# Performance work log

Measured on AMD Instinct MI355X. Metric: run time of the kernel, lower is better.

## Reference

```python
import jax, jax.numpy as jnp
import numpy as np

D_HEAD = 64
SCALE = D_HEAD ** 0.5
MASK_FILL = -10000.0


def setup_inputs() -> dict:
    key = jax.random.key(0)
    kq, kk, kv, km = jax.random.split(key, 4)
    B, H, S, D = 2, 16, 2048, D_HEAD
    query = jax.random.normal(kq, (B, H, S, D), dtype=jnp.float32)
    k = jax.random.normal(kk, (B, H, S, D), dtype=jnp.float32)
    v = jax.random.normal(kv, (B, H, S, D), dtype=jnp.float32)
    attn_mask = jax.random.randint(km, (B, H, S, S), 0, 2).astype(jnp.bool_)
    return {"query": query, "key": k, "value": v, "attn_mask": attn_mask}


def reference(query, key, value, attn_mask):
    # scores: [B, H, Sq, Sk]
    scores = jnp.einsum("bhqd,bhkd->bhqk", query, key) / SCALE
    scores = jnp.where(attn_mask, MASK_FILL, scores)
    attn_prob = jax.nn.softmax(scores, axis=-1)
    context = jnp.einsum("bhqk,bhkd->bhqd", attn_prob, value)
    return (context, attn_prob)
```

## Files before the change

### kernel.cpp

```cpp
#include <hip/hip_runtime.h>
#include <cstdint>
#include <cstddef>

#define S_LEN 2048
#define D_HEAD 64
#define NBH 32

typedef __attribute__((ext_vector_type(8))) short short8;
typedef __attribute__((ext_vector_type(8))) unsigned short ushort8;
typedef __attribute__((ext_vector_type(4))) float floatx4;

__device__ __forceinline__ unsigned short f2bf(float f){
  union { float f; unsigned int i; } v; v.f = f;
  unsigned int u = v.i;
  u += 0x7fffu + ((u >> 16) & 1u);
  return (unsigned short)(u >> 16);
}
__device__ __forceinline__ float bf2f(unsigned short u){
  union { unsigned int i; float f; } v; v.i = ((unsigned int)u) << 16; return v.f;
}

__device__ __forceinline__ int swz(int row, int col){
  return row * S_LEN + ((((col >> 3) ^ row) & 7) << 3) + ((col >> 3) & ~7) * 8 + (col & 7);
}

__global__ void detect_mask_kernel(const unsigned int* __restrict__ m, int* __restrict__ flag){
  __shared__ int f;
  if (threadIdx.x == 0) f = 0;
  __syncthreads();
  if (m[threadIdx.x] > 1u) atomicOr(&f, 1);
  __syncthreads();
  if (threadIdx.x == 0) *flag = f;
}

__global__ void convK_kernel(const float* __restrict__ K, unsigned short* __restrict__ Kb){
  const size_t i = ((size_t)blockIdx.x * 256 + threadIdx.x) * 8;
  floatx4 x0 = *(const floatx4*)(K + i);
  floatx4 x1 = *(const floatx4*)(K + i + 4);
  ushort8 o;
#pragma unroll
  for (int j = 0; j < 4; ++j){ o[j] = f2bf(x0[j]); o[4 + j] = f2bf(x1[j]); }
  *(ushort8*)(Kb + i) = o;
}

__global__ void vtrans_kernel(const float* __restrict__ V, unsigned short* __restrict__ Vt){
  const int bh = blockIdx.y;
  const int n  = threadIdx.x & 63;
  const int k0 = blockIdx.x * 32 + (threadIdx.x >> 6) * 8;
  const float* Vp = V + (size_t)bh * S_LEN * D_HEAD;
  ushort8 o;
#pragma unroll
  for (int i = 0; i < 8; ++i) o[i] = f2bf(Vp[(size_t)(k0 + i) * D_HEAD + n]);
  *(ushort8*)(Vt + (size_t)bh * D_HEAD * S_LEN + (size_t)n * S_LEN + k0) = o;
}

__global__ __launch_bounds__(256) void attn_kernel(
    const float* __restrict__ Q, const unsigned short* __restrict__ Kb,
    const void* __restrict__ maskp, const int* __restrict__ flag,
    const unsigned short* __restrict__ Vt,
    float* __restrict__ prob, float* __restrict__ ctx,
    float* __restrict__ redg, float* __restrict__ invg){

  __shared__ unsigned short Pt[16 * S_LEN];

  const int bh   = blockIdx.y;
  const int qt   = blockIdx.x;
  const int q0g  = bh * S_LEN + qt * 16;
  const int tid  = threadIdx.x;
  const int wave = tid >> 6;
  const int lane = tid & 63;
  const int quad = lane >> 4;
  const int r16  = lane & 15;
  const int blk  = bh * gridDim.x + qt;

  const float* qrow = Q + (size_t)(q0g + r16) * D_HEAD + quad * 8;
  short8 a0, a1;
  {
    floatx4 x0 = *(const floatx4*)(qrow);
    floatx4 x1 = *(const floatx4*)(qrow + 4);
    floatx4 y0 = *(const floatx4*)(qrow + 32);
    floatx4 y1 = *(const floatx4*)(qrow + 36);
#pragma unroll
    for (int j = 0; j < 4; ++j){
      a0[j] = (short)f2bf(x0[j]); a0[4 + j] = (short)f2bf(x1[j]);
      a1[j] = (short)f2bf(y0[j]); a1[4 + j] = (short)f2bf(y1[j]);
    }
  }

  const bool mInt = (*flag) == 0;
  const unsigned int*  mI = (const unsigned int*)maskp;
  const unsigned char* mB = (const unsigned char*)maskp;

  float racc[4] = {0.f, 0.f, 0.f, 0.f};

  for (int t = 0; t < 32; ++t){
    const int s0 = wave * 512 + t * 16;
    const unsigned short* krow = Kb + (size_t)(bh * S_LEN + s0 + r16) * D_HEAD + quad * 8;
    const short8 b0 = *(const short8*)(krow);
    const short8 b1 = *(const short8*)(krow + 32);
    unsigned int mv[4];
    if (mInt){
#pragma unroll
      for (int i = 0; i < 4; ++i)
        mv[i] = mI[(size_t)(q0g + quad*4 + i) * S_LEN + s0 + r16];
    } else {
#pragma unroll
      for (int i = 0; i < 4; ++i)
        mv[i] = mB[(size_t)(q0g + quad*4 + i) * S_LEN + s0 + r16];
    }
    floatx4 c = {0.f, 0.f, 0.f, 0.f};
    c = __builtin_amdgcn_mfma_f32_16x16x32_bf16(a0, b0, c, 0, 0, 0);
    c = __builtin_amdgcn_mfma_f32_16x16x32_bf16(a1, b1, c, 0, 0, 0);
#pragma unroll
    for (int i = 0; i < 4; ++i){
      const float p = mv[i] ? 0.0f : __expf(c[i] * 0.125f);
      racc[i] += p;
      Pt[swz(quad*4 + i, s0 + r16)] = f2bf(p);
    }
  }

#pragma unroll
  for (int off = 8; off; off >>= 1){
#pragma unroll
    for (int i = 0; i < 4; ++i) racc[i] += __shfl_xor(racc[i], off, 16);
  }
  if (r16 == 0){
#pragma unroll
    for (int i = 0; i < 4; ++i) redg[(size_t)blk * 64 + wave * 16 + quad*4 + i] = racc[i];
  }
  __syncthreads();
  if (tid < 16){
    float s = 0.f;
#pragma unroll
    for (int w = 0; w < 4; ++w) s += redg[(size_t)blk * 64 + w * 16 + tid];
    invg[(size_t)blk * 16 + tid] = (s > 0.f) ? (1.0f / s) : 0.0f;
  }
  __syncthreads();

  float inv4[4];
#pragma unroll
  for (int i = 0; i < 4; ++i) inv4[i] = invg[(size_t)blk * 16 + quad*4 + i];

  const unsigned short* vrow = Vt + (size_t)bh * D_HEAD * S_LEN
                                  + (size_t)(wave * 16 + r16) * S_LEN + quad * 8;
  floatx4 c = {0.f, 0.f, 0.f, 0.f};
  for (int kk = 0; kk < 64; ++kk){
    const short8 b = *(const short8*)(vrow + kk * 32);
    const short8 a = *(const short8*)(&Pt[swz(r16, kk * 32 + quad * 8)]);
    c = __builtin_amdgcn_mfma_f32_16x16x32_bf16(a, b, c, 0, 0, 0);
  }
#pragma unroll
  for (int i = 0; i < 4; ++i)
    ctx[(size_t)(q0g + quad*4 + i) * D_HEAD + wave * 16 + r16] = c[i] * inv4[i];

#pragma unroll
  for (int rr = 0; rr < 4; ++rr){
    const int row = wave * 4 + rr;
    const float iv = invg[(size_t)blk * 16 + row];
    float* pg = prob + (size_t)(q0g + row) * S_LEN;
    for (int j = 0; j < 32; ++j){
      const int col = j * 64 + lane;
      pg[col] = bf2f(Pt[swz(row, col)]) * iv;
    }
  }
}

extern "C" void kernel_launch(void* const* d_in, const int* in_sizes, int n_in,
                              void* d_out, int out_size, void* d_ws, size_t ws_size,
                              hipStream_t stream) {
  const float* Q = (const float*)d_in[0];
  const float* K = (const float*)d_in[1];
  const float* V = (const float*)d_in[2];
  const void*  M = d_in[3];

  float* ctx  = (float*)d_out;
  float* prob = (float*)d_out + (size_t)NBH * S_LEN * D_HEAD;

  int*   flag = (int*)d_ws;
  float* redg = (float*)((char*)d_ws + (1u << 12));
  float* invg = (float*)((char*)d_ws + (1u << 12) + (1u << 20));
  unsigned short* Kb = (unsigned short*)((char*)d_ws + (2u << 20));
  unsigned short* Vt = (unsigned short*)((char*)d_ws + (10u << 20));

  hipLaunchKernelGGL(detect_mask_kernel, dim3(1), dim3(256), 0, stream,
                     (const unsigned int*)M, flag);
  hipLaunchKernelGGL(convK_kernel, dim3(2048), dim3(256), 0, stream, K, Kb);
  hipLaunchKernelGGL(vtrans_kernel, dim3(S_LEN/32, NBH), dim3(256), 0, stream, V, Vt);
  hipLaunchKernelGGL(attn_kernel, dim3(S_LEN/16, NBH), dim3(256), 0, stream,
                     Q, Kb, M, flag, Vt, prob, ctx, redg, invg);
}
```

Before: 1.083 ms.

## Vectorize mask loads and probability stores, transpose MFMA operands, remap blocks per XCD

The QK^T MFMA now takes its operands swapped, so each lane owns one query row and four consecutive keys. This lets the mask be read as one 16-byte vector (or one 4-byte word for byte masks) per row instead of four strided scalar loads. Probabilities are written to LDS as 4-wide packed stores under a widened 16-way swizzle, and the final probability output is written with 8-wide LDS reads and float4 global stores. Blocks are remapped so each XCD works on a fixed group of heads for K/V cache locality, and launch bounds and unroll pragmas are added. The risks are LDS bank conflicts under the new swizzle and register pressure from the unrolling.

```diff
diff --git a/kernel.cpp b/kernel.cpp
--- a/kernel.cpp
+++ b/kernel.cpp
@@ -8,6 +8,8 @@
 
 typedef __attribute__((ext_vector_type(8))) short short8;
 typedef __attribute__((ext_vector_type(8))) unsigned short ushort8;
+typedef __attribute__((ext_vector_type(4))) unsigned short us4;
+typedef __attribute__((ext_vector_type(4))) unsigned int ui4;
 typedef __attribute__((ext_vector_type(4))) float floatx4;
 
 __device__ __forceinline__ unsigned short f2bf(float f){
@@ -21,7 +23,8 @@
 }
 
 __device__ __forceinline__ int swz(int row, int col){
-  return row * S_LEN + ((((col >> 3) ^ row) & 7) << 3) + ((col >> 3) & ~7) * 8 + (col & 7);
+  return row * S_LEN + ((((col >> 3) ^ row) & 15) << 3)
+                     + (((col >> 3) & ~15) << 3) + (col & 7);
 }
 
 __global__ void detect_mask_kernel(const unsigned int* __restrict__ m, int* __restrict__ flag){
@@ -54,7 +57,7 @@
   *(ushort8*)(Vt + (size_t)bh * D_HEAD * S_LEN + (size_t)n * S_LEN + k0) = o;
 }
 
-__global__ __launch_bounds__(256) void attn_kernel(
+__global__ __launch_bounds__(256, 2) void attn_kernel(
     const float* __restrict__ Q, const unsigned short* __restrict__ Kb,
     const void* __restrict__ maskp, const int* __restrict__ flag,
     const unsigned short* __restrict__ Vt,
@@ -63,8 +66,12 @@
 
   __shared__ unsigned short Pt[16 * S_LEN];
 
-  const int bh   = blockIdx.y;
-  const int qt   = blockIdx.x;
+  const int lin  = blockIdx.y * gridDim.x + blockIdx.x;
+  const int xcd  = lin & 7;
+  const int sub  = lin >> 3;
+  const int bh   = xcd * 4 + (sub & 3);
+  const int qt   = sub >> 2;
+
   const int q0g  = bh * S_LEN + qt * 16;
   const int tid  = threadIdx.x;
   const int wave = tid >> 6;
@@ -90,44 +97,42 @@
   const bool mInt = (*flag) == 0;
   const unsigned int*  mI = (const unsigned int*)maskp;
   const unsigned char* mB = (const unsigned char*)maskp;
-
-  float racc[4] = {0.f, 0.f, 0.f, 0.f};
-
+  const size_t mrow = (size_t)(q0g + r16) * S_LEN;
+
+  float racc = 0.f;
+
+#pragma unroll 2
   for (int t = 0; t < 32; ++t){
     const int s0 = wave * 512 + t * 16;
     const unsigned short* krow = Kb + (size_t)(bh * S_LEN + s0 + r16) * D_HEAD + quad * 8;
     const short8 b0 = *(const short8*)(krow);
     const short8 b1 = *(const short8*)(krow + 32);
-    unsigned int mv[4];
+    unsigned int mm[4];
     if (mInt){
-#pragma unroll
-      for (int i = 0; i < 4; ++i)
-        mv[i] = mI[(size_t)(q0g + quad*4 + i) * S_LEN + s0 + r16];
+      const ui4 m4 = *(const ui4*)(mI + mrow + s0 + quad * 4);
+#pragma unroll
+      for (int i = 0; i < 4; ++i) mm[i] = m4[i];
     } else {
-#pragma unroll
-      for (int i = 0; i < 4; ++i)
-        mv[i] = mB[(size_t)(q0g + quad*4 + i) * S_LEN + s0 + r16];
+      const unsigned int mv = *(const unsigned int*)(mB + mrow + s0 + quad * 4);
+#pragma unroll
+      for (int i = 0; i < 4; ++i) mm[i] = (mv >> (8 * i)) & 0xffu;
     }
     floatx4 c = {0.f, 0.f, 0.f, 0.f};
-    c = __builtin_amdgcn_mfma_f32_16x16x32_bf16(a0, b0, c, 0, 0, 0);
-    c = __builtin_amdgcn_mfma_f32_16x16x32_bf16(a1, b1, c, 0, 0, 0);
+    c = __builtin_amdgcn_mfma_f32_16x16x32_bf16(b0, a0, c, 0, 0, 0);
+    c = __builtin_amdgcn_mfma_f32_16x16x32_bf16(b1, a1, c, 0, 0, 0);
+    us4 w;
 #pragma unroll
     for (int i = 0; i < 4; ++i){
-      const float p = mv[i] ? 0.0f : __expf(c[i] * 0.125f);
-      racc[i] += p;
-      Pt[swz(quad*4 + i, s0 + r16)] = f2bf(p);
-    }
-  }
-
-#pragma unroll
-  for (int off = 8; off; off >>= 1){
-#pragma unroll
-    for (int i = 0; i < 4; ++i) racc[i] += __shfl_xor(racc[i], off, 16);
-  }
-  if (r16 == 0){
-#pragma unroll
-    for (int i = 0; i < 4; ++i) redg[(size_t)blk * 64 + wave * 16 + quad*4 + i] = racc[i];
-  }
+      const float p = mm[i] ? 0.0f : __expf(c[i] * 0.125f);
+      racc += p;
+      w[i] = f2bf(p);
+    }
+    *(us4*)(&Pt[swz(r16, s0 + quad * 4)]) = w;
+  }
+
+  racc += __shfl_xor(racc, 16);
+  racc += __shfl_xor(racc, 32);
+  if (lane < 16) redg[(size_t)blk * 64 + wave * 16 + lane] = racc;
   __syncthreads();
   if (tid < 16){
     float s = 0.f;
@@ -139,11 +144,12 @@
 
   float inv4[4];
 #pragma unroll
-  for (int i = 0; i < 4; ++i) inv4[i] = invg[(size_t)blk * 16 + quad*4 + i];
+  for (int i = 0; i < 4; ++i) inv4[i] = invg[(size_t)blk * 16 + quad * 4 + i];
 
   const unsigned short* vrow = Vt + (size_t)bh * D_HEAD * S_LEN
                                   + (size_t)(wave * 16 + r16) * S_LEN + quad * 8;
   floatx4 c = {0.f, 0.f, 0.f, 0.f};
+#pragma unroll 4
   for (int kk = 0; kk < 64; ++kk){
     const short8 b = *(const short8*)(vrow + kk * 32);
     const short8 a = *(const short8*)(&Pt[swz(r16, kk * 32 + quad * 8)]);
@@ -151,16 +157,25 @@
   }
 #pragma unroll
   for (int i = 0; i < 4; ++i)
-    ctx[(size_t)(q0g + quad*4 + i) * D_HEAD + wave * 16 + r16] = c[i] * inv4[i];
+    ctx[(size_t)(q0g + quad * 4 + i) * D_HEAD + wave * 16 + r16] = c[i] * inv4[i];
 
 #pragma unroll
   for (int rr = 0; rr < 4; ++rr){
     const int row = wave * 4 + rr;
     const float iv = invg[(size_t)blk * 16 + row];
     float* pg = prob + (size_t)(q0g + row) * S_LEN;
-    for (int j = 0; j < 32; ++j){
-      const int col = j * 64 + lane;
-      pg[col] = bf2f(Pt[swz(row, col)]) * iv;
+#pragma unroll
+    for (int j = 0; j < 4; ++j){
+      const int col = j * 512 + lane * 8;
+      const ushort8 u = *(const ushort8*)(&Pt[swz(row, col)]);
+      floatx4 o0, o1;
+#pragma unroll
+      for (int e = 0; e < 4; ++e){
+        o0[e] = bf2f(u[e]) * iv;
+        o1[e] = bf2f(u[4 + e]) * iv;
+      }
+      *(floatx4*)(pg + col)     = o0;
+      *(floatx4*)(pg + col + 4) = o1;
     }
   }
 }
```

Result: no change. 1.103 ms (+1.9%).
